# Optimization experiments

Measured on AMD Instinct MI355X. Metric: run time of the kernel, lower is better.

Reference implementation:

```python
import jax, jax.numpy as jnp
import numpy as np

H1, W1GRID, K_SIZE, B = 28, 28, 5, 512
K2 = K_SIZE * K_SIZE  # 25 kernel weight matrices
_BITS = np.array([[0, 0], [0, 1], [1, 0], [1, 1]])  # 2^dim basis combos


def _grid_edges(h, w):
    """8-neighborhood grid graph; returns (src, dst, pseudo in [0,1]^2)."""
    ys, xs = np.meshgrid(np.arange(h), np.arange(w), indexing='ij')
    node = (ys * w + xs).reshape(-1)
    ys, xs = ys.reshape(-1), xs.reshape(-1)
    srcs, dsts, pses = [], [], []
    for dy in (-1, 0, 1):
        for dx in (-1, 0, 1):
            if dy == 0 and dx == 0:
                continue
            ny, nx = ys + dy, xs + dx
            ok = (ny >= 0) & (ny < h) & (nx >= 0) & (nx < w)
            srcs.append((ny * w + nx)[ok])   # neighbor j
            dsts.append(node[ok])            # center i
            p = np.array([[(dx + 1) / 2.0, (dy + 1) / 2.0]], dtype=np.float32)
            pses.append(np.repeat(p, ok.sum(), axis=0))
    return (np.concatenate(srcs), np.concatenate(dsts), np.concatenate(pses))


def _batched_graph(h, w, batch):
    s, d, p = _grid_edges(h, w)
    n = h * w
    off = (np.arange(batch, dtype=np.int64) * n)[:, None]
    src = (s[None, :] + off).reshape(-1)
    dst = (d[None, :] + off).reshape(-1)
    pse = np.tile(p, (batch, 1))
    return np.stack([src, dst]), pse


def setup_inputs() -> dict:
    key = jax.random.key(0)
    ks = jax.random.split(key, 8)
    e1, p1 = _batched_graph(28, 28, B)
    e2, p2 = _batched_graph(14, 14, B)
    return {
        'x': jax.random.uniform(ks[0], (B * 784, 1), jnp.float32),
        'pseudo1': jnp.asarray(p1), 'pseudo2': jnp.asarray(p2),
        'W1': jax.random.normal(ks[1], (K2, 1, 32), jnp.float32) * 0.2,
        'root1': jax.random.normal(ks[2], (1, 32), jnp.float32) * 0.2,
        'b1': jnp.zeros((32,), jnp.float32),
        'W2': jax.random.normal(ks[3], (K2, 32, 64), jnp.float32) * 0.05,
        'root2': jax.random.normal(ks[4], (32, 64), jnp.float32) * 0.05,
        'b2': jnp.zeros((64,), jnp.float32),
        'fc1_w': jax.random.normal(ks[5], (3136, 512), jnp.float32) * 0.02,
        'fc1_b': jnp.zeros((512,), jnp.float32),
        'fc2_w': jax.random.normal(ks[6], (512, 10), jnp.float32) * 0.05,
        'fc2_b': jnp.zeros((10,), jnp.float32),
        'edge_index1': jnp.asarray(e1, jnp.int64 if jax.config.jax_enable_x64 else jnp.int32),
        'edge_index2': jnp.asarray(e2, jnp.int64 if jax.config.jax_enable_x64 else jnp.int32),
    }


def _spline_basis(pseudo, k):
    # open B-spline, degree 1: each dim contributes 2 knots with linear weights
    frac = pseudo * (k - 1)                                   # [E,2]
    lo = jnp.clip(jnp.floor(frac), 0, k - 2)
    f = frac - lo                                             # [E,2]
    w = jnp.stack([1.0 - f, f], axis=-1)                      # [E,2,2]
    idx = jnp.stack([lo, lo + 1], axis=-1).astype(jnp.int32)  # [E,2,2]
    basis = w[:, 0, _BITS[:, 0]] * w[:, 1, _BITS[:, 1]]       # [E,4]
    widx = idx[:, 0, _BITS[:, 0]] + idx[:, 1, _BITS[:, 1]] * k  # [E,4]
    return basis, widx


def _spline_conv(x, edge_index, pseudo, W, root, bias, n_nodes, k):
    src, dst = edge_index[0], edge_index[1]
    x_j = x[src]                                              # [E,Cin] gather
    basis, widx = _spline_basis(pseudo, k)                    # [E,4]
    kk = k * k
    flat = (dst[:, None] * kk + widx).reshape(-1)             # [E*4]
    contrib = (basis[:, :, None] * x_j[:, None, :]).reshape(-1, x.shape[1])
    S = jnp.zeros((n_nodes * kk, x.shape[1]), x.dtype).at[flat].add(contrib)
    S = S.reshape(n_nodes, kk, x.shape[1])                    # per-node per-kernel sums
    deg = jnp.zeros((n_nodes,), x.dtype).at[dst].add(1.0)
    out = jnp.einsum('nki,kio->no', S, W) / jnp.maximum(deg, 1.0)[:, None]
    return out + x @ root + bias


def _pool2x2(x, b, hw, c):
    return x.reshape(b, hw // 2, 2, hw // 2, 2, c).max(axis=(2, 4))


def reference(x, pseudo1, pseudo2, W1, root1, b1, W2, root2, b2,
              fc1_w, fc1_b, fc2_w, fc2_b, edge_index1, edge_index2):
    n1 = x.shape[0]
    b = n1 // 784
    h = jax.nn.elu(_spline_conv(x, edge_index1, pseudo1, W1, root1, b1, n1, K_SIZE))
    h = _pool2x2(h, b, 28, 32).reshape(-1, 32)                # [B*196,32]
    h = jax.nn.elu(_spline_conv(h, edge_index2, pseudo2, W2, root2, b2, b * 196, K_SIZE))
    h = _pool2x2(h, b, 14, 64).reshape(-1, 7 * 7 * 64)        # [B,3136]
    h = jax.nn.elu(h @ fc1_w + fc1_b)
    # dropout is identity in eval mode
    h = jax.nn.elu(h @ fc2_w + fc2_b)
    return jax.nn.log_softmax(h, axis=-1)
```

## Files before the change

kernel.cpp:

```cpp
#include <hip/hip_runtime.h>
#include <math.h>

#define BATCH 512

__device__ __forceinline__ float elu1(float v) {
    return v > 0.f ? v : expm1f(v);
}

__global__ __launch_bounds__(256) void k1_conv1_pool(
    const float* __restrict__ x, const float* __restrict__ W1,
    const float* __restrict__ root1, const float* __restrict__ b1,
    float* __restrict__ p1) {
    __shared__ float xs[900];
    __shared__ float w1s[8 * 32 + 64];
    const int b = blockIdx.x;
    const int t = threadIdx.x;

    for (int l = t; l < 900; l += 256) xs[l] = 0.f;
    {
        int d = t >> 5, c = t & 31;
        int e = d + (d >= 4 ? 1 : 0);
        int dy = e / 3 - 1, dx = e % 3 - 1;
        int widx = 2 * (dx + 1) + 10 * (dy + 1);
        w1s[t] = W1[widx * 32 + c];
        if (t < 32) { w1s[256 + t] = root1[t]; w1s[288 + t] = b1[t]; }
    }
    __syncthreads();
    const float* xb = x + (size_t)b * 784;
    for (int l = t; l < 784; l += 256) {
        int y = l / 28, xx = l % 28;
        xs[(y + 1) * 30 + xx + 1] = xb[l];
    }
    __syncthreads();

    if (t >= 196) return;
    int py = t / 14, px = t % 14;
    int xbse[4];
    float xc[4], inv[4];
    #pragma unroll
    for (int p = 0; p < 4; ++p) {
        int sy = p >> 1, sx = p & 1;
        int y = 2 * py + sy, xx = 2 * px + sx;
        xbse[p] = (y + 1) * 30 + xx + 1;
        xc[p] = xs[xbse[p]];
        int nvy = 3 - (y == 0) - (y == 27);
        int nvx = 3 - (xx == 0) - (xx == 27);
        inv[p] = 1.f / (float)(nvy * nvx - 1);
    }
    const float4* w4 = (const float4*)w1s;
    float* outp = p1 + ((size_t)b * 196 + t) * 32;

    #pragma unroll
    for (int h = 0; h < 2; ++h) {
        float4 acc[4][4];
        #pragma unroll
        for (int p = 0; p < 4; ++p)
            #pragma unroll
            for (int q = 0; q < 4; ++q) acc[p][q] = make_float4(0.f, 0.f, 0.f, 0.f);
        #pragma unroll
        for (int d = 0; d < 8; ++d) {
            int e = d + (d >= 4 ? 1 : 0);
            int od = (e / 3 - 1) * 30 + (e % 3 - 1);
            float4 w0 = w4[d * 8 + h * 4 + 0];
            float4 w1 = w4[d * 8 + h * 4 + 1];
            float4 w2 = w4[d * 8 + h * 4 + 2];
            float4 w3 = w4[d * 8 + h * 4 + 3];
            #pragma unroll
            for (int p = 0; p < 4; ++p) {
                float xv = xs[xbse[p] + od];
                acc[p][0].x += xv * w0.x; acc[p][0].y += xv * w0.y; acc[p][0].z += xv * w0.z; acc[p][0].w += xv * w0.w;
                acc[p][1].x += xv * w1.x; acc[p][1].y += xv * w1.y; acc[p][1].z += xv * w1.z; acc[p][1].w += xv * w1.w;
                acc[p][2].x += xv * w2.x; acc[p][2].y += xv * w2.y; acc[p][2].z += xv * w2.z; acc[p][2].w += xv * w2.w;
                acc[p][3].x += xv * w3.x; acc[p][3].y += xv * w3.y; acc[p][3].z += xv * w3.z; acc[p][3].w += xv * w3.w;
            }
        }
        #pragma unroll
        for (int q = 0; q < 4; ++q) {
            float4 rt = w4[64 + h * 4 + q];
            float4 bs = w4[72 + h * 4 + q];
            float4 m = make_float4(-1e30f, -1e30f, -1e30f, -1e30f);
            #pragma unroll
            for (int p = 0; p < 4; ++p) {
                float4 v;
                v.x = elu1(acc[p][q].x * inv[p] + xc[p] * rt.x + bs.x);
                v.y = elu1(acc[p][q].y * inv[p] + xc[p] * rt.y + bs.y);
                v.z = elu1(acc[p][q].z * inv[p] + xc[p] * rt.z + bs.z);
                v.w = elu1(acc[p][q].w * inv[p] + xc[p] * rt.w + bs.w);
                m.x = fmaxf(m.x, v.x); m.y = fmaxf(m.y, v.y);
                m.z = fmaxf(m.z, v.z); m.w = fmaxf(m.w, v.w);
            }
            *(float4*)(outp + h * 16 + q * 4) = m;
        }
    }
}

__global__ __launch_bounds__(256) void k2_conv2_pool(
    const float* __restrict__ p1, const float* __restrict__ W2,
    const float* __restrict__ root2, const float* __restrict__ b2,
    float* __restrict__ p2) {
    __shared__ float xs[9216];
    __shared__ float wb[2][1152];
    const int b = blockIdx.x >> 1, h = blockIdx.x & 1;
    const int t = threadIdx.x;
    const int cell = t >> 2, cg = t & 3;
    const int coff = cg * 8;

    static const int widx_t[8] = {0, 2, 4, 10, 14, 20, 22, 24};

    const int wi = t >> 3, wc8 = t & 7;
    const size_t wsrc = (size_t)wi * 64 + h * 32 + wc8 * 4;
    {
        float4 v = *(const float4*)(W2 + wsrc);
        *(float4*)(wb[0] + wi * 36 + wc8 * 4) = v;
    }
    for (int l = t; l < 9216; l += 256) xs[l] = 0.f;
    __syncthreads();
    {
        const float* src = p1 + (size_t)b * 6272;
        for (int l = t; l < 6272; l += 256) {
            int node = l >> 5, i = l & 31;
            int y = node / 14, xx = node - y * 14;
            int np = (y + 1) * 16 + xx + 1;
            xs[np * 36 + 4 * ((i >> 2) ^ ((np >> 4) & 7)) + (i & 3)] = src[l];
        }
    }
    __syncthreads();

    const int ccell = (cell < 49) ? cell : 48;
    const int py = ccell / 7, px = ccell - py * 7;
    int npv[4];
    float inv[4];
    #pragma unroll
    for (int p = 0; p < 4; ++p) {
        int sy = p >> 1, sx = p & 1;
        int y = 2 * py + sy, xx = 2 * px + sx;
        npv[p] = (y + 1) * 16 + xx + 1;
        int nvy = 3 - (y == 0) - (y == 13);
        int nvx = 3 - (xx == 0) - (xx == 13);
        inv[p] = 1.f / (float)(nvy * nvx - 1);
    }

    float4 acc[4][2];
    #pragma unroll
    for (int p = 0; p < 4; ++p) { acc[p][0] = make_float4(0,0,0,0); acc[p][1] = make_float4(0,0,0,0); }

    for (int d = 0; d < 9; ++d) {
        float4 pf;
        if (d < 8) {
            int nd = d + 1;
            const float* nsrc = (nd == 8) ? root2 : (W2 + (size_t)widx_t[nd] * 2048);
            pf = *(const float4*)(nsrc + wsrc);
        }
        if (d == 8) {
            #pragma unroll
            for (int p = 0; p < 4; ++p) {
                acc[p][0].x *= inv[p]; acc[p][0].y *= inv[p]; acc[p][0].z *= inv[p]; acc[p][0].w *= inv[p];
                acc[p][1].x *= inv[p]; acc[p][1].y *= inv[p]; acc[p][1].z *= inv[p]; acc[p][1].w *= inv[p];
            }
        }
        int dnode = 0;
        if (d < 8) {
            int e = d + (d >= 4 ? 1 : 0);
            dnode = (e / 3 - 1) * 16 + (e % 3 - 1);
        }
        int xb0, xb1, xb2, xb3, sz0, sz1, sz2, sz3;
        {
            int n0 = npv[0] + dnode, n1 = npv[1] + dnode,
                n2 = npv[2] + dnode, n3 = npv[3] + dnode;
            xb0 = n0 * 36; sz0 = (n0 >> 4) & 7;
            xb1 = n1 * 36; sz1 = (n1 >> 4) & 7;
            xb2 = n2 * 36; sz2 = (n2 >> 4) & 7;
            xb3 = n3 * 36; sz3 = (n3 >> 4) & 7;
        }
        const float* wcur = wb[d & 1] + coff;
        #pragma unroll 2
        for (int i4 = 0; i4 < 8; ++i4) {
            float4 xv0 = *(const float4*)(xs + xb0 + 4 * (i4 ^ sz0));
            float4 xv1 = *(const float4*)(xs + xb1 + 4 * (i4 ^ sz1));
            float4 xv2 = *(const float4*)(xs + xb2 + 4 * (i4 ^ sz2));
            float4 xv3 = *(const float4*)(xs + xb3 + 4 * (i4 ^ sz3));
            float xa0[4] = {xv0.x, xv0.y, xv0.z, xv0.w};
            float xa1[4] = {xv1.x, xv1.y, xv1.z, xv1.w};
            float xa2[4] = {xv2.x, xv2.y, xv2.z, xv2.w};
            float xa3[4] = {xv3.x, xv3.y, xv3.z, xv3.w};
            #pragma unroll
            for (int ii = 0; ii < 4; ++ii) {
                const float* wrow = wcur + (i4 * 4 + ii) * 36;
                float4 w0 = *(const float4*)(wrow + 0);
                float4 w1 = *(const float4*)(wrow + 4);
                float x0 = xa0[ii], x1 = xa1[ii], x2 = xa2[ii], x3 = xa3[ii];
                acc[0][0].x += x0 * w0.x; acc[0][0].y += x0 * w0.y; acc[0][0].z += x0 * w0.z; acc[0][0].w += x0 * w0.w;
                acc[0][1].x += x0 * w1.x; acc[0][1].y += x0 * w1.y; acc[0][1].z += x0 * w1.z; acc[0][1].w += x0 * w1.w;
                acc[1][0].x += x1 * w0.x; acc[1][0].y += x1 * w0.y; acc[1][0].z += x1 * w0.z; acc[1][0].w += x1 * w0.w;
                acc[1][1].x += x1 * w1.x; acc[1][1].y += x1 * w1.y; acc[1][1].z += x1 * w1.z; acc[1][1].w += x1 * w1.w;
                acc[2][0].x += x2 * w0.x; acc[2][0].y += x2 * w0.y; acc[2][0].z += x2 * w0.z; acc[2][0].w += x2 * w0.w;
                acc[2][1].x += x2 * w1.x; acc[2][1].y += x2 * w1.y; acc[2][1].z += x2 * w1.z; acc[2][1].w += x2 * w1.w;
                acc[3][0].x += x3 * w0.x; acc[3][0].y += x3 * w0.y; acc[3][0].z += x3 * w0.z; acc[3][0].w += x3 * w0.w;
                acc[3][1].x += x3 * w1.x; acc[3][1].y += x3 * w1.y; acc[3][1].z += x3 * w1.z; acc[3][1].w += x3 * w1.w;
            }
        }
        if (d < 8) {
            *(float4*)(wb[(d + 1) & 1] + wi * 36 + wc8 * 4) = pf;
        }
        __syncthreads();
    }

    if (cell < 49) {
        float* outp = p2 + (size_t)b * 3136 + cell * 64 + h * 32 + cg * 8;
        #pragma unroll
        for (int q = 0; q < 2; ++q) {
            float4 bs = *(const float4*)(b2 + h * 32 + cg * 8 + q * 4);
            float4 m = make_float4(-1e30f, -1e30f, -1e30f, -1e30f);
            #pragma unroll
            for (int p = 0; p < 4; ++p) {
                float4 v;
                v.x = elu1(acc[p][q].x + bs.x);
                v.y = elu1(acc[p][q].y + bs.y);
                v.z = elu1(acc[p][q].z + bs.z);
                v.w = elu1(acc[p][q].w + bs.w);
                m.x = fmaxf(m.x, v.x); m.y = fmaxf(m.y, v.y);
                m.z = fmaxf(m.z, v.z); m.w = fmaxf(m.w, v.w);
            }
            *(float4*)(outp + q * 4) = m;
        }
    }
}

__global__ __launch_bounds__(256) void k3a_fc1(
    const float* __restrict__ A, const float* __restrict__ B,
    float* __restrict__ part) {
    __shared__ float As[2][16][64];
    __shared__ float Bs[2][16][72];
    const int t = threadIdx.x;
    const int tx = t & 15, ty = t >> 4;
    const int n0 = blockIdx.x * 64, m0 = blockIdx.y * 64;
    const int k0 = blockIdx.z * 272;
    const int steps = ((blockIdx.z == 11) ? 144 : 272) >> 4;

    const int sm = t & 63, k4 = t >> 6;
    const int sk = t >> 4, sc = t & 15;
    const float* Ap = A + (size_t)(m0 + sm) * 3136 + k0 + k4 * 4;
    const float* Bp = B + (size_t)(k0 + sk) * 512 + n0 + sc * 4;

    {
        float4 av = *(const float4*)Ap;
        float4 bv = *(const float4*)Bp;
        As[0][k4 * 4 + 0][sm] = av.x; As[0][k4 * 4 + 1][sm] = av.y;
        As[0][k4 * 4 + 2][sm] = av.z; As[0][k4 * 4 + 3][sm] = av.w;
        *(float4*)&Bs[0][sk][sc * 4] = bv;
    }
    __syncthreads();

    float acc[4][4];
    #pragma unroll
    for (int r = 0; r < 4; ++r)
        #pragma unroll
        for (int c = 0; c < 4; ++c) acc[r][c] = 0.f;

    for (int s = 0; s < steps; ++s) {
        float4 a0, b0;
        if (s + 1 < steps) {
            a0 = *(const float4*)(Ap + (s + 1) * 16);
            b0 = *(const float4*)(Bp + (size_t)(s + 1) * 16 * 512);
        }
        const int cur = s & 1;
        #pragma unroll
        for (int k = 0; k < 16; ++k) {
            float4 a4 = *(const float4*)&As[cur][k][ty * 4];
            float4 b4 = *(const float4*)&Bs[cur][k][tx * 4];
            acc[0][0] += a4.x * b4.x; acc[0][1] += a4.x * b4.y; acc[0][2] += a4.x * b4.z; acc[0][3] += a4.x * b4.w;
            acc[1][0] += a4.y * b4.x; acc[1][1] += a4.y * b4.y; acc[1][2] += a4.y * b4.z; acc[1][3] += a4.y * b4.w;
            acc[2][0] += a4.z * b4.x; acc[2][1] += a4.z * b4.y; acc[2][2] += a4.z * b4.z; acc[2][3] += a4.z * b4.w;
            acc[3][0] += a4.w * b4.x; acc[3][1] += a4.w * b4.y; acc[3][2] += a4.w * b4.z; acc[3][3] += a4.w * b4.w;
        }
        if (s + 1 < steps) {
            const int nxt = cur ^ 1;
            As[nxt][k4 * 4 + 0][sm] = a0.x; As[nxt][k4 * 4 + 1][sm] = a0.y;
            As[nxt][k4 * 4 + 2][sm] = a0.z; As[nxt][k4 * 4 + 3][sm] = a0.w;
            *(float4*)&Bs[nxt][sk][sc * 4] = b0;
        }
        __syncthreads();
    }

    float* pbase = part + ((size_t)blockIdx.z * 512 + m0 + ty * 4) * 512 + n0;
    #pragma unroll
    for (int r = 0; r < 4; ++r)
        *(float4*)(pbase + (size_t)r * 512 + tx * 4) =
            make_float4(acc[r][0], acc[r][1], acc[r][2], acc[r][3]);
}

__global__ __launch_bounds__(256) void k34_reduce_fc2_lsm(
    const float* __restrict__ part, const float* __restrict__ fc1b,
    const float* __restrict__ w, const float* __restrict__ fc2b,
    float* __restrict__ out, int KZ) {
    __shared__ float red[4][10];
    const int b = blockIdx.x, t = threadIdx.x;

    float a0 = fc1b[t], a1 = fc1b[t + 256];
    for (int kz = 0; kz < KZ; ++kz) {
        const float* pr = part + ((size_t)kz * 512 + b) * 512;
        a0 += pr[t]; a1 += pr[t + 256];
    }
    a0 = elu1(a0); a1 = elu1(a1);

    float acc[10];
    #pragma unroll
    for (int o = 0; o < 10; ++o)
        acc[o] = a0 * w[t * 10 + o] + a1 * w[(t + 256) * 10 + o];
    #pragma unroll
    for (int s = 32; s; s >>= 1)
        #pragma unroll
        for (int o = 0; o < 10; ++o) acc[o] += __shfl_xor(acc[o], s, 64);
    if ((t & 63) == 0) {
        #pragma unroll
        for (int o = 0; o < 10; ++o) red[t >> 6][o] = acc[o];
    }
    __syncthreads();
    if (t == 0) {
        float v[10], m = -1e30f;
        #pragma unroll
        for (int o = 0; o < 10; ++o) {
            float s = red[0][o] + red[1][o] + red[2][o] + red[3][o] + fc2b[o];
            v[o] = elu1(s);
            m = fmaxf(m, v[o]);
        }
        float ssum = 0.f;
        #pragma unroll
        for (int o = 0; o < 10; ++o) ssum += expf(v[o] - m);
        float lse = m + logf(ssum);
        #pragma unroll
        for (int o = 0; o < 10; ++o) out[(size_t)b * 10 + o] = v[o] - lse;
    }
}

extern "C" void kernel_launch(void* const* d_in, const int* in_sizes, int n_in,
                              void* d_out, int out_size, void* d_ws, size_t ws_size,
                              hipStream_t stream) {
    const float* x     = (const float*)d_in[0];
    const float* W1    = (const float*)d_in[3];
    const float* root1 = (const float*)d_in[4];
    const float* b1v   = (const float*)d_in[5];
    const float* W2    = (const float*)d_in[6];
    const float* root2 = (const float*)d_in[7];
    const float* b2v   = (const float*)d_in[8];
    const float* fc1w  = (const float*)d_in[9];
    const float* fc1b  = (const float*)d_in[10];
    const float* fc2w  = (const float*)d_in[11];
    const float* fc2b  = (const float*)d_in[12];

    float* ws = (float*)d_ws;
    float* p1 = ws;
    float* p2 = p1 + (size_t)BATCH * 196 * 32;
    float* part = p1;

    k1_conv1_pool<<<dim3(BATCH), 256, 0, stream>>>(x, W1, root1, b1v, p1);
    k2_conv2_pool<<<dim3(2 * BATCH), 256, 0, stream>>>(p1, W2, root2, b2v, p2);
    k3a_fc1<<<dim3(8, 8, 12), 256, 0, stream>>>(p2, fc1w, part);
    k34_reduce_fc2_lsm<<<dim3(BATCH), 256, 0, stream>>>(part, fc1b, fc2w, fc2b, (float*)d_out, 12);
}
```

Before: 128.9 us.

## Retile conv2 to one block per sample and read fc1 weights from global

The conv2 kernel now runs one block per sample covering all 64 output channels, instead of two blocks each doing half the channels. Each thread computes a 2x4 node tile over 8 channels, so every x-tile shared-memory load is reused across more FMAs and the input is staged only once per sample. The fc1 kernel stops staging B in shared memory and reads the weight rows directly from global/L1, which cuts LDS traffic but relies on cache hits. The risks are higher register pressure from 64 accumulators per thread, fewer blocks in conv2, and wasted threads in the clamped tiles.

```diff
diff --git a/kernel.cpp b/kernel.cpp
--- a/kernel.cpp
+++ b/kernel.cpp
@@ -99,19 +99,21 @@
     const float* __restrict__ root2, const float* __restrict__ b2,
     float* __restrict__ p2) {
     __shared__ float xs[9216];
-    __shared__ float wb[2][1152];
-    const int b = blockIdx.x >> 1, h = blockIdx.x & 1;
+    __shared__ float wb[2][2304];
+    const int b = blockIdx.x;
     const int t = threadIdx.x;
-    const int cell = t >> 2, cg = t & 3;
-    const int coff = cg * 8;
+    int tile = t >> 3; if (tile > 27) tile = 27;
+    const int cg = t & 7;
 
     static const int widx_t[8] = {0, 2, 4, 10, 14, 20, 22, 24};
-
-    const int wi = t >> 3, wc8 = t & 7;
-    const size_t wsrc = (size_t)wi * 64 + h * 32 + wc8 * 4;
+    static const int ddy[8] = {-1,-1,-1, 0, 0, 1, 1, 1};
+    static const int ddx[8] = {-1, 0, 1,-1, 1,-1, 0, 1};
+
     {
-        float4 v = *(const float4*)(W2 + wsrc);
-        *(float4*)(wb[0] + wi * 36 + wc8 * 4) = v;
+        const float4* s4 = (const float4*)W2;
+        float4 v0 = s4[t], v1 = s4[t + 256];
+        *(float4*)(wb[0] + (t >> 4) * 72 + (t & 15) * 4) = v0;
+        *(float4*)(wb[0] + ((t + 256) >> 4) * 72 + (t & 15) * 4) = v1;
     }
     for (int l = t; l < 9216; l += 256) xs[l] = 0.f;
     __syncthreads();
@@ -126,102 +128,105 @@
     }
     __syncthreads();
 
-    const int ccell = (cell < 49) ? cell : 48;
-    const int py = ccell / 7, px = ccell - py * 7;
-    int npv[4];
-    float inv[4];
-    #pragma unroll
-    for (int p = 0; p < 4; ++p) {
-        int sy = p >> 1, sx = p & 1;
-        int y = 2 * py + sy, xx = 2 * px + sx;
-        npv[p] = (y + 1) * 16 + xx + 1;
-        int nvy = 3 - (y == 0) - (y == 13);
-        int nvx = 3 - (xx == 0) - (xx == 13);
-        inv[p] = 1.f / (float)(nvy * nvx - 1);
-    }
-
-    float4 acc[4][2];
-    #pragma unroll
-    for (int p = 0; p < 4; ++p) { acc[p][0] = make_float4(0,0,0,0); acc[p][1] = make_float4(0,0,0,0); }
+    const int py = tile >> 2, q = tile & 3;
+    int npb[8]; float invd[8];
+    #pragma unroll
+    for (int p = 0; p < 8; ++p) {
+        int r = p >> 2, c = p & 3;
+        int gy = 2 * py + r, gx = 4 * q + c;
+        npb[p] = (gy + 1) * 16 + gx + 1;
+        int gxc = gx > 13 ? 13 : gx;
+        int nvy = 3 - (gy == 0) - (gy == 13);
+        int nvx = 3 - (gxc == 0) - (gxc == 13);
+        invd[p] = 1.f / (float)(nvy * nvx - 1);
+    }
+
+    float4 acc[8][2];
+    #pragma unroll
+    for (int p = 0; p < 8; ++p) { acc[p][0] = make_float4(0,0,0,0); acc[p][1] = make_float4(0,0,0,0); }
 
     for (int d = 0; d < 9; ++d) {
-        float4 pf;
+        float4 pf0, pf1;
         if (d < 8) {
-            int nd = d + 1;
-            const float* nsrc = (nd == 8) ? root2 : (W2 + (size_t)widx_t[nd] * 2048);
-            pf = *(const float4*)(nsrc + wsrc);
+            const float* nsrc = (d + 1 == 8) ? root2 : (W2 + (size_t)widx_t[d + 1] * 2048);
+            pf0 = ((const float4*)nsrc)[t];
+            pf1 = ((const float4*)nsrc)[t + 256];
         }
         if (d == 8) {
             #pragma unroll
-            for (int p = 0; p < 4; ++p) {
-                acc[p][0].x *= inv[p]; acc[p][0].y *= inv[p]; acc[p][0].z *= inv[p]; acc[p][0].w *= inv[p];
-                acc[p][1].x *= inv[p]; acc[p][1].y *= inv[p]; acc[p][1].z *= inv[p]; acc[p][1].w *= inv[p];
-            }
-        }
-        int dnode = 0;
-        if (d < 8) {
-            int e = d + (d >= 4 ? 1 : 0);
-            dnode = (e / 3 - 1) * 16 + (e % 3 - 1);
-        }
-        int xb0, xb1, xb2, xb3, sz0, sz1, sz2, sz3;
-        {
-            int n0 = npv[0] + dnode, n1 = npv[1] + dnode,
-                n2 = npv[2] + dnode, n3 = npv[3] + dnode;
-            xb0 = n0 * 36; sz0 = (n0 >> 4) & 7;
-            xb1 = n1 * 36; sz1 = (n1 >> 4) & 7;
-            xb2 = n2 * 36; sz2 = (n2 >> 4) & 7;
-            xb3 = n3 * 36; sz3 = (n3 >> 4) & 7;
-        }
-        const float* wcur = wb[d & 1] + coff;
+            for (int p = 0; p < 8; ++p) {
+                acc[p][0].x *= invd[p]; acc[p][0].y *= invd[p]; acc[p][0].z *= invd[p]; acc[p][0].w *= invd[p];
+                acc[p][1].x *= invd[p]; acc[p][1].y *= invd[p]; acc[p][1].z *= invd[p]; acc[p][1].w *= invd[p];
+            }
+        }
+        int dnode = (d < 8) ? (ddy[d] * 16 + ddx[d]) : 0;
+        int ax[8], sz[8];
+        #pragma unroll
+        for (int p = 0; p < 8; ++p) {
+            int np = npb[p] + dnode;
+            ax[p] = np * 36;
+            sz[p] = (np >> 4) & 7;
+        }
+        const float* wcur = wb[d & 1];
         #pragma unroll 2
         for (int i4 = 0; i4 < 8; ++i4) {
-            float4 xv0 = *(const float4*)(xs + xb0 + 4 * (i4 ^ sz0));
-            float4 xv1 = *(const float4*)(xs + xb1 + 4 * (i4 ^ sz1));
-            float4 xv2 = *(const float4*)(xs + xb2 + 4 * (i4 ^ sz2));
-            float4 xv3 = *(const float4*)(xs + xb3 + 4 * (i4 ^ sz3));
-            float xa0[4] = {xv0.x, xv0.y, xv0.z, xv0.w};
-            float xa1[4] = {xv1.x, xv1.y, xv1.z, xv1.w};
-            float xa2[4] = {xv2.x, xv2.y, xv2.z, xv2.w};
-            float xa3[4] = {xv3.x, xv3.y, xv3.z, xv3.w};
+            float xa[8][4];
+            #pragma unroll
+            for (int p = 0; p < 8; ++p) {
+                float4 v = *(const float4*)(xs + ax[p] + 4 * (i4 ^ sz[p]));
+                xa[p][0] = v.x; xa[p][1] = v.y; xa[p][2] = v.z; xa[p][3] = v.w;
+            }
             #pragma unroll
             for (int ii = 0; ii < 4; ++ii) {
-                const float* wrow = wcur + (i4 * 4 + ii) * 36;
-                float4 w0 = *(const float4*)(wrow + 0);
-                float4 w1 = *(const float4*)(wrow + 4);
-                float x0 = xa0[ii], x1 = xa1[ii], x2 = xa2[ii], x3 = xa3[ii];
-                acc[0][0].x += x0 * w0.x; acc[0][0].y += x0 * w0.y; acc[0][0].z += x0 * w0.z; acc[0][0].w += x0 * w0.w;
-                acc[0][1].x += x0 * w1.x; acc[0][1].y += x0 * w1.y; acc[0][1].z += x0 * w1.z; acc[0][1].w += x0 * w1.w;
-                acc[1][0].x += x1 * w0.x; acc[1][0].y += x1 * w0.y; acc[1][0].z += x1 * w0.z; acc[1][0].w += x1 * w0.w;
-                acc[1][1].x += x1 * w1.x; acc[1][1].y += x1 * w1.y; acc[1][1].z += x1 * w1.z; acc[1][1].w += x1 * w1.w;
-                acc[2][0].x += x2 * w0.x; acc[2][0].y += x2 * w0.y; acc[2][0].z += x2 * w0.z; acc[2][0].w += x2 * w0.w;
-                acc[2][1].x += x2 * w1.x; acc[2][1].y += x2 * w1.y; acc[2][1].z += x2 * w1.z; acc[2][1].w += x2 * w1.w;
-                acc[3][0].x += x3 * w0.x; acc[3][0].y += x3 * w0.y; acc[3][0].z += x3 * w0.z; acc[3][0].w += x3 * w0.w;
-                acc[3][1].x += x3 * w1.x; acc[3][1].y += x3 * w1.y; acc[3][1].z += x3 * w1.z; acc[3][1].w += x3 * w1.w;
+                const float* wr = wcur + (i4 * 4 + ii) * 72 + cg * 8;
+                float4 w0 = *(const float4*)wr;
+                float4 w1 = *(const float4*)(wr + 4);
+                #pragma unroll
+                for (int p = 0; p < 8; ++p) {
+                    float xv = xa[p][ii];
+                    acc[p][0].x += xv * w0.x; acc[p][0].y += xv * w0.y;
+                    acc[p][0].z += xv * w0.z; acc[p][0].w += xv * w0.w;
+                    acc[p][1].x += xv * w1.x; acc[p][1].y += xv * w1.y;
+                    acc[p][1].z += xv * w1.z; acc[p][1].w += xv * w1.w;
+                }
             }
         }
         if (d < 8) {
-            *(float4*)(wb[(d + 1) & 1] + wi * 36 + wc8 * 4) = pf;
+            float* wn = wb[(d + 1) & 1];
+            *(float4*)(wn + (t >> 4) * 72 + (t & 15) * 4) = pf0;
+            *(float4*)(wn + ((t + 256) >> 4) * 72 + (t & 15) * 4) = pf1;
         }
         __syncthreads();
     }
 
-    if (cell < 49) {
-        float* outp = p2 + (size_t)b * 3136 + cell * 64 + h * 32 + cg * 8;
-        #pragma unroll
-        for (int q = 0; q < 2; ++q) {
-            float4 bs = *(const float4*)(b2 + h * 32 + cg * 8 + q * 4);
-            float4 m = make_float4(-1e30f, -1e30f, -1e30f, -1e30f);
-            #pragma unroll
-            for (int p = 0; p < 4; ++p) {
-                float4 v;
-                v.x = elu1(acc[p][q].x + bs.x);
-                v.y = elu1(acc[p][q].y + bs.y);
-                v.z = elu1(acc[p][q].z + bs.z);
-                v.w = elu1(acc[p][q].w + bs.w);
-                m.x = fmaxf(m.x, v.x); m.y = fmaxf(m.y, v.y);
-                m.z = fmaxf(m.z, v.z); m.w = fmaxf(m.w, v.w);
-            }
-            *(float4*)(outp + q * 4) = m;
+    if (t < 224) {
+        float4 bs0 = *(const float4*)(b2 + cg * 8);
+        float4 bs1 = *(const float4*)(b2 + cg * 8 + 4);
+        float* outb = p2 + (size_t)b * 3136;
+        #pragma unroll
+        for (int cc = 0; cc < 2; ++cc) {
+            int cellcol = 2 * q + cc;
+            if (cellcol > 6) continue;
+            float4 m0 = make_float4(-1e30f,-1e30f,-1e30f,-1e30f);
+            float4 m1 = m0;
+            #pragma unroll
+            for (int r = 0; r < 2; ++r)
+            #pragma unroll
+            for (int c2 = 0; c2 < 2; ++c2) {
+                int p = r * 4 + cc * 2 + c2;
+                float4 v0, v1;
+                v0.x = elu1(acc[p][0].x + bs0.x); v0.y = elu1(acc[p][0].y + bs0.y);
+                v0.z = elu1(acc[p][0].z + bs0.z); v0.w = elu1(acc[p][0].w + bs0.w);
+                v1.x = elu1(acc[p][1].x + bs1.x); v1.y = elu1(acc[p][1].y + bs1.y);
+                v1.z = elu1(acc[p][1].z + bs1.z); v1.w = elu1(acc[p][1].w + bs1.w);
+                m0.x = fmaxf(m0.x, v0.x); m0.y = fmaxf(m0.y, v0.y);
+                m0.z = fmaxf(m0.z, v0.z); m0.w = fmaxf(m0.w, v0.w);
+                m1.x = fmaxf(m1.x, v1.x); m1.y = fmaxf(m1.y, v1.y);
+                m1.z = fmaxf(m1.z, v1.z); m1.w = fmaxf(m1.w, v1.w);
+            }
+            int cell = py * 7 + cellcol;
+            *(float4*)(outb + cell * 64 + cg * 8)     = m0;
+            *(float4*)(outb + cell * 64 + cg * 8 + 4) = m1;
         }
     }
 }
@@ -229,25 +234,21 @@
 __global__ __launch_bounds__(256) void k3a_fc1(
     const float* __restrict__ A, const float* __restrict__ B,
     float* __restrict__ part) {
-    __shared__ float As[2][16][64];
-    __shared__ float Bs[2][16][72];
+    __shared__ float As[2][16][68];
     const int t = threadIdx.x;
     const int tx = t & 15, ty = t >> 4;
-    const int n0 = blockIdx.x * 64, m0 = blockIdx.y * 64;
-    const int k0 = blockIdx.z * 272;
-    const int steps = ((blockIdx.z == 11) ? 144 : 272) >> 4;
-
+    const int n0 = blockIdx.x * 64, m0 = blockIdx.y * 64, kz = blockIdx.z;
+    const int k0 = kz * 272;
+    const int steps = ((kz == 11) ? 144 : 272) >> 4;
     const int sm = t & 63, k4 = t >> 6;
-    const int sk = t >> 4, sc = t & 15;
+
     const float* Ap = A + (size_t)(m0 + sm) * 3136 + k0 + k4 * 4;
-    const float* Bp = B + (size_t)(k0 + sk) * 512 + n0 + sc * 4;
+    const float* Bp = B + (size_t)k0 * 512 + n0 + tx * 4;
 
     {
         float4 av = *(const float4*)Ap;
-        float4 bv = *(const float4*)Bp;
         As[0][k4 * 4 + 0][sm] = av.x; As[0][k4 * 4 + 1][sm] = av.y;
         As[0][k4 * 4 + 2][sm] = av.z; As[0][k4 * 4 + 3][sm] = av.w;
-        *(float4*)&Bs[0][sk][sc * 4] = bv;
     }
     __syncthreads();
 
@@ -257,17 +258,14 @@
         #pragma unroll
         for (int c = 0; c < 4; ++c) acc[r][c] = 0.f;
 
+    int cur = 0;
     for (int s = 0; s < steps; ++s) {
-        float4 a0, b0;
-        if (s + 1 < steps) {
-            a0 = *(const float4*)(Ap + (s + 1) * 16);
-            b0 = *(const float4*)(Bp + (size_t)(s + 1) * 16 * 512);
-        }
-        const int cur = s & 1;
+        float4 anext;
+        if (s + 1 < steps) anext = *(const float4*)(Ap + (s + 1) * 16);
         #pragma unroll
         for (int k = 0; k < 16; ++k) {
             float4 a4 = *(const float4*)&As[cur][k][ty * 4];
-            float4 b4 = *(const float4*)&Bs[cur][k][tx * 4];
+            float4 b4 = *(const float4*)(Bp + (size_t)(s * 16 + k) * 512);
             acc[0][0] += a4.x * b4.x; acc[0][1] += a4.x * b4.y; acc[0][2] += a4.x * b4.z; acc[0][3] += a4.x * b4.w;
             acc[1][0] += a4.y * b4.x; acc[1][1] += a4.y * b4.y; acc[1][2] += a4.y * b4.z; acc[1][3] += a4.y * b4.w;
             acc[2][0] += a4.z * b4.x; acc[2][1] += a4.z * b4.y; acc[2][2] += a4.z * b4.z; acc[2][3] += a4.z * b4.w;
@@ -275,14 +273,14 @@
         }
         if (s + 1 < steps) {
             const int nxt = cur ^ 1;
-            As[nxt][k4 * 4 + 0][sm] = a0.x; As[nxt][k4 * 4 + 1][sm] = a0.y;
-            As[nxt][k4 * 4 + 2][sm] = a0.z; As[nxt][k4 * 4 + 3][sm] = a0.w;
-            *(float4*)&Bs[nxt][sk][sc * 4] = b0;
+            As[nxt][k4 * 4 + 0][sm] = anext.x; As[nxt][k4 * 4 + 1][sm] = anext.y;
+            As[nxt][k4 * 4 + 2][sm] = anext.z; As[nxt][k4 * 4 + 3][sm] = anext.w;
+            cur = nxt;
         }
         __syncthreads();
     }
 
-    float* pbase = part + ((size_t)blockIdx.z * 512 + m0 + ty * 4) * 512 + n0;
+    float* pbase = part + ((size_t)kz * 512 + m0 + ty * 4) * 512 + n0;
     #pragma unroll
     for (int r = 0; r < 4; ++r)
         *(float4*)(pbase + (size_t)r * 512 + tx * 4) =
@@ -354,7 +352,7 @@
     float* part = p1;
 
     k1_conv1_pool<<<dim3(BATCH), 256, 0, stream>>>(x, W1, root1, b1v, p1);
-    k2_conv2_pool<<<dim3(2 * BATCH), 256, 0, stream>>>(p1, W2, root2, b2v, p2);
+    k2_conv2_pool<<<dim3(BATCH), 256, 0, stream>>>(p1, W2, root2, b2v, p2);
     k3a_fc1<<<dim3(8, 8, 12), 256, 0, stream>>>(p2, fc1w, part);
     k34_reduce_fc2_lsm<<<dim3(BATCH), 256, 0, stream>>>(part, fc1b, fc2w, fc2b, (float*)d_out, 12);
 }
```

After: 134.5 us. 4.4% more time.
